# Kernel tuning notes

Hardware: AMD Instinct MI355X
Metric: run time of the kernel (lower is better)

## Reference

```python
import jax, jax.numpy as jnp
import numpy as np

N = 43
H = N // 2  # 21


def _mk(key, i, o):
    kw, kb = jax.random.split(key)
    bound = 1.0 / np.sqrt(i)
    W = jax.random.uniform(kw, (i, o), jnp.float32, -bound, bound)
    b = jax.random.uniform(kb, (o,), jnp.float32, -bound, bound)
    return W, b


def setup_inputs() -> dict:
    key = jax.random.key(0)
    keys = jax.random.split(key, 11)
    x = jax.random.normal(keys[0], (1048576, N), jnp.float32)
    dims = [(N, N), (N, N), (N, N), (N, N), (N, H),  # encoder
            (H, N), (N, N), (N, N), (N, N), (N, N)]  # decoder
    out = {"x": x}
    for li, (i, o) in enumerate(dims):
        W, b = _mk(keys[li + 1], i, o)
        out[f"W{li}"] = W
        out[f"b{li}"] = b
    return out


def reference(x, W0, b0, W1, b1, W2, b2, W3, b3, W4, b4,
              W5, b5, W6, b6, W7, b7, W8, b8, W9, b9):
    Ws = [W0, W1, W2, W3, W4, W5, W6, W7, W8, W9]
    bs = [b0, b1, b2, b3, b4, b5, b6, b7, b8, b9]
    h = x
    for li in range(10):
        h = h @ Ws[li] + bs[li]
        # tanh after every layer except encoder bottleneck (4) and final (9)
        if li not in (4, 9):
            h = jnp.tanh(h)
    return h
```

## Files before the change

### kernel.cpp

```cpp
#include <hip/hip_runtime.h>


typedef __fp16 pk16x2 __attribute__((ext_vector_type(2)));
typedef _Float16 f16x8 __attribute__((ext_vector_type(8)));
typedef float f32x4 __attribute__((ext_vector_type(4)));
typedef unsigned u32x4 __attribute__((ext_vector_type(4)));

#define TPB 1024
#define NBLK 256
#define ITERS 8
#define NROWS 1048576
#define NCOL 43
#define ROWB 172u
#define XBYTES ((size_t)NROWS * ROWB)
#define WSTRIDE 72
#define SLOT_ROWS 44
#define WSLOT (SLOT_ROWS * WSTRIDE)
#define W_BYTES (10 * WSLOT * 2)
#define XBUF_BYTES 6144
#define X_BASE W_BYTES
#define SMEM_BYTES (X_BASE + 16 * XBUF_BYTES + 64)

__device__ __forceinline__ float fast_tanh(float x) {
  float t = __builtin_amdgcn_exp2f(x * 2.8853900817779268f);
  float r = __builtin_amdgcn_rcpf(t + 1.0f);
  return __builtin_fmaf(-2.0f, r, 1.0f);
}

__device__ __forceinline__ unsigned pk2(float a, float b) {
  pk16x2 h = __builtin_amdgcn_cvt_pkrtz(a, b);
  return __builtin_bit_cast(unsigned, h);
}

struct FragsV { f16x8 s0c0, s0c1, s1c0, s1c1; };

template <int NT, int KC, bool DOTANH, int NLOUT, int KCN>
__device__ __forceinline__ FragsV layer_fwd(const _Float16* __restrict__ Wl,
                                            FragsV Bi, f32x4 Z, int g, int lr) {
  f16x8 Bv[2][2];
  Bv[0][0] = Bi.s0c0; Bv[0][1] = Bi.s0c1;
  Bv[1][0] = Bi.s1c0; Bv[1][1] = Bi.s1c1;

  f32x4 acc[3][2];
#pragma unroll
  for (int t = 0; t < NT; ++t) {
    f16x8 A = *(const f16x8*)(Wl + (16 * t + lr) * WSTRIDE + 8 * g);
#pragma unroll
    for (int s = 0; s < 2; ++s)
      acc[t][s] = __builtin_amdgcn_mfma_f32_16x16x32_f16(A, Bv[s][0], Z,
                                                         0, 0, 0);
  }
#pragma unroll
  for (int c = 1; c < KC; ++c)
#pragma unroll
    for (int t = 0; t < NT; ++t) {
      f16x8 A = *(const f16x8*)(Wl + (16 * t + lr) * WSTRIDE + 8 * g + 32 * c);
#pragma unroll
      for (int s = 0; s < 2; ++s)
        acc[t][s] = __builtin_amdgcn_mfma_f32_16x16x32_f16(A, Bv[s][c],
                                                           acc[t][s], 0, 0, 0);
    }

  f16x8 oc0[2], oc1[2];
#pragma unroll
  for (int s = 0; s < 2; ++s) {
    unsigned pk[3][2];
#pragma unroll
    for (int t = 0; t < NT; ++t) {
      float v[4];
#pragma unroll
      for (int r = 0; r < 4; ++r) {
        float u = acc[t][s][r];
        if (DOTANH) u = fast_tanh(u);
        if (t == (NLOUT >> 4)) {
          int col = 16 * t + 4 * g + r;
          u = (col == NLOUT) ? 1.0f : u;
        }
        v[r] = u;
      }
      pk[t][0] = pk2(v[0], v[1]);
      pk[t][1] = pk2(v[2], v[3]);
    }
    u32x4 d0 = {pk[0][0], pk[0][1], pk[1][0], pk[1][1]};
    oc0[s] = __builtin_bit_cast(f16x8, d0);
    if (KCN == 2) {
      u32x4 d1 = {pk[NT - 1][0], pk[NT - 1][1], 0u, 0u};
      oc1[s] = __builtin_bit_cast(f16x8, d1);
    } else {
      oc1[s] = oc0[s];
    }
  }
  FragsV O;
  O.s0c0 = oc0[0]; O.s0c1 = oc1[0];
  O.s1c0 = oc0[1]; O.s1c1 = oc1[1];
  return O;
}

extern "C" __global__ void __launch_bounds__(TPB)
ae_kernel(const float* __restrict__ x,
          const float* __restrict__ W0, const float* __restrict__ B0,
          const float* __restrict__ W1, const float* __restrict__ B1,
          const float* __restrict__ W2, const float* __restrict__ B2,
          const float* __restrict__ W3, const float* __restrict__ B3,
          const float* __restrict__ W4, const float* __restrict__ B4,
          const float* __restrict__ W5, const float* __restrict__ B5,
          const float* __restrict__ W6, const float* __restrict__ B6,
          const float* __restrict__ W7, const float* __restrict__ B7,
          const float* __restrict__ W8, const float* __restrict__ B8,
          const float* __restrict__ W9, const float* __restrict__ B9,
          float* __restrict__ out) {
  extern __shared__ char smem[];
  _Float16* lw = (_Float16*)smem;

  const int tid = threadIdx.x;
  const int wave = tid >> 6;
  const int lane = tid & 63;
  const int g = lane >> 4;
  const int lr = lane & 15;

  {
    const float* Wp[10] = {W0, W1, W2, W3, W4, W5, W6, W7, W8, W9};
    const float* Bp[10] = {B0, B1, B2, B3, B4, B5, B6, B7, B8, B9};
    const int KLs[10] = {43, 43, 43, 43, 43, 21, 43, 43, 43, 43};
    const int NLs[10] = {43, 43, 43, 43, 21, 43, 43, 43, 43, 43};
#pragma unroll
    for (int L = 0; L < 10; ++L) {
      const float* Wl = Wp[L];
      const float* Bl = Bp[L];
      const int KL = KLs[L], NL = NLs[L];
      for (int idx = tid; idx < SLOT_ROWS * 64; idx += TPB) {
        int n = idx >> 6, kp = idx & 63;
        float v = 0.0f;
        if (n < NL) {
          int c = kp >> 5, g2 = (kp >> 3) & 3, j = kp & 7;
          int F;
          if (L == 0) F = kp;
          else if (c == 0) F = 16 * (j >> 2) + 4 * g2 + (j & 3);
          else if (j < 4)  F = 32 + 4 * g2 + j;
          else             F = 63;
          if (F < KL) v = Wl[F * NL + n];
          else if (F == KL) v = Bl[n];
        }
        lw[L * WSLOT + n * WSTRIDE + kp] = (_Float16)v;
      }
    }
  }

  unsigned dmaoff[6];
#pragma unroll
  for (int i = 0; i < 6; ++i) {
    unsigned u = 64u * i + (unsigned)lane;
    dmaoff[i] = (u / 12u) * ROWB + (u % 12u) * 16u;
  }

  __syncthreads();

  const char* xc = (const char*)x;
  const char* xlim = xc + (XBYTES - 16);
  const unsigned blockbase = (unsigned)blockIdx.x * (ITERS * 512) + wave * 32;
  float* xb = (float*)(smem + X_BASE + wave * XBUF_BYTES);
  const f32x4 Z = {0.f, 0.f, 0.f, 0.f};

  {
    const char* base = xc + blockbase * ROWB;
#pragma unroll
    for (int i = 0; i < 6; ++i) {
      const char* src = base + dmaoff[i];
      src = (src > xlim) ? xlim : src;
      __builtin_amdgcn_global_load_lds(
          (const __attribute__((address_space(1))) void*)src,
          (__attribute__((address_space(3))) void*)((char*)xb + i * 1024),
          16, 0, 0);
    }
  }

#pragma unroll 1
  for (int it = 0; it < ITERS; ++it) {
    const unsigned row0 = blockbase + (unsigned)it * 512u;

    asm volatile("s_waitcnt vmcnt(0)" ::: "memory");

    FragsV B;
#pragma unroll
    for (int s = 0; s < 2; ++s) {
      const float* xr = xb + (16 * s + lr) * 48;
      f32x4 q0 = *(const f32x4*)(xr + 8 * g);
      f32x4 q1 = *(const f32x4*)(xr + 8 * g + 4);
      f32x4 q2 = *(const f32x4*)(xr + 32 + 8 * g);
      f32x4 q3 = *(const f32x4*)(xr + 36 + 8 * g);
      float e3 = (g == 1) ? 1.0f : q2[3];
      u32x4 d0 = {pk2(q0[0], q0[1]), pk2(q0[2], q0[3]),
                  pk2(q1[0], q1[1]), pk2(q1[2], q1[3])};
      u32x4 d1 = {pk2(q2[0], q2[1]), pk2(q2[2], e3),
                  pk2(q3[0], q3[1]), pk2(q3[2], q3[3])};
      if (s == 0) { B.s0c0 = __builtin_bit_cast(f16x8, d0);
                    B.s0c1 = __builtin_bit_cast(f16x8, d1); }
      else        { B.s1c0 = __builtin_bit_cast(f16x8, d0);
                    B.s1c1 = __builtin_bit_cast(f16x8, d1); }
    }

    asm volatile("s_waitcnt lgkmcnt(0)" ::: "memory");
    if (it + 1 < ITERS) {
      const char* base = xc + (row0 + 512u) * ROWB;
#pragma unroll
      for (int i = 0; i < 6; ++i) {
        const char* src = base + dmaoff[i];
        src = (src > xlim) ? xlim : src;
        __builtin_amdgcn_global_load_lds(
            (const __attribute__((address_space(1))) void*)src,
            (__attribute__((address_space(3))) void*)((char*)xb + i * 1024),
            16, 0, 0);
      }
    }

    B = layer_fwd<3, 2, true, 43, 2>(lw + 0 * WSLOT, B, Z, g, lr);
    B = layer_fwd<3, 2, true, 43, 2>(lw + 1 * WSLOT, B, Z, g, lr);
    B = layer_fwd<3, 2, true, 43, 2>(lw + 2 * WSLOT, B, Z, g, lr);
    B = layer_fwd<3, 2, true, 43, 2>(lw + 3 * WSLOT, B, Z, g, lr);
    B = layer_fwd<2, 2, false, 21, 1>(lw + 4 * WSLOT, B, Z, g, lr);
    B = layer_fwd<3, 1, true, 43, 2>(lw + 5 * WSLOT, B, Z, g, lr);
    B = layer_fwd<3, 2, true, 43, 2>(lw + 6 * WSLOT, B, Z, g, lr);
    B = layer_fwd<3, 2, true, 43, 2>(lw + 7 * WSLOT, B, Z, g, lr);
    B = layer_fwd<3, 2, true, 43, 2>(lw + 8 * WSLOT, B, Z, g, lr);

    {
      f16x8 Bv[2][2];
      Bv[0][0] = B.s0c0; Bv[0][1] = B.s0c1;
      Bv[1][0] = B.s1c0; Bv[1][1] = B.s1c1;
      f32x4 a9[3][2];
#pragma unroll
      for (int t = 0; t < 3; ++t) {
        f16x8 A = *(const f16x8*)(lw + 9 * WSLOT + (16 * t + lr) * WSTRIDE +
                                  8 * g);
#pragma unroll
        for (int s = 0; s < 2; ++s)
          a9[t][s] = __builtin_amdgcn_mfma_f32_16x16x32_f16(A, Bv[s][0], Z,
                                                            0, 0, 0);
      }
#pragma unroll
      for (int t = 0; t < 3; ++t) {
        f16x8 A = *(const f16x8*)(lw + 9 * WSLOT + (16 * t + lr) * WSTRIDE +
                                  8 * g + 32);
#pragma unroll
        for (int s = 0; s < 2; ++s)
          a9[t][s] = __builtin_amdgcn_mfma_f32_16x16x32_f16(A, Bv[s][1],
                                                            a9[t][s], 0, 0, 0);
      }
      char* ob = (char*)out + ((size_t)(row0 + lr) * ROWB + 16u * g);
#pragma unroll
      for (int t = 0; t < 3; ++t)
#pragma unroll
        for (int s = 0; s < 2; ++s)
#pragma unroll
          for (int r = 0; r < 4; ++r) {
            if (t < 2 || 4 * g + r < 11)
              *(float*)(ob + 2752 * s + 64 * t + 4 * r) = a9[t][s][r];
          }
    }
  }
}

extern "C" void kernel_launch(void* const* d_in, const int* in_sizes, int n_in,
                              void* d_out, int out_size, void* d_ws,
                              size_t ws_size, hipStream_t stream) {
  const float* x = (const float*)d_in[0];
  const float* W[10];
  const float* B[10];
  for (int i = 0; i < 10; ++i) {
    W[i] = (const float*)d_in[1 + 2 * i];
    B[i] = (const float*)d_in[2 + 2 * i];
  }
  (void)hipFuncSetAttribute(reinterpret_cast<const void*>(ae_kernel),
                            hipFuncAttributeMaxDynamicSharedMemorySize,
                            SMEM_BYTES);
  ae_kernel<<<dim3(NBLK), dim3(TPB), SMEM_BYTES, stream>>>(
      x, W[0], B[0], W[1], B[1], W[2], B[2], W[3], B[3], W[4], B[4],
      W[5], B[5], W[6], B[6], W[7], B[7], W[8], B[8], W[9], B[9],
      (float*)d_out);
}
```

Baseline: 137.5 us.

## Prefetch next layer's weight fragments from LDS and tighten the x staging layout

```diff
diff --git a/kernel.cpp b/kernel.cpp
--- a/kernel.cpp
+++ b/kernel.cpp
@@ -17,9 +17,11 @@
 #define SLOT_ROWS 44
 #define WSLOT (SLOT_ROWS * WSTRIDE)
 #define W_BYTES (10 * WSLOT * 2)
+#define W_PAD 640
+#define XROWF 44
 #define XBUF_BYTES 6144
-#define X_BASE W_BYTES
-#define SMEM_BYTES (X_BASE + 16 * XBUF_BYTES + 64)
+#define X_BASE (W_BYTES + W_PAD)
+#define SMEM_BYTES (X_BASE + 16 * XBUF_BYTES)
 
 __device__ __forceinline__ float fast_tanh(float x) {
   float t = __builtin_amdgcn_exp2f(x * 2.8853900817779268f);
@@ -33,33 +35,51 @@
 }
 
 struct FragsV { f16x8 s0c0, s0c1, s1c0, s1c1; };
+struct A6 { f16x8 m0, m1, m2, m3, m4, m5; };
+
+template <int NT, int KC>
+__device__ __forceinline__ A6 load_A(const _Float16* __restrict__ Wl,
+                                     int g, int lr) {
+  A6 a;
+  const _Float16* p = Wl + lr * WSTRIDE + 8 * g;
+  a.m0 = *(const f16x8*)(p);
+  if constexpr (NT > 1) a.m1 = *(const f16x8*)(p + 16 * WSTRIDE);
+  if constexpr (NT > 2) a.m2 = *(const f16x8*)(p + 32 * WSTRIDE);
+  if constexpr (KC > 1) {
+    a.m3 = *(const f16x8*)(p + 32);
+    if constexpr (NT > 1) a.m4 = *(const f16x8*)(p + 16 * WSTRIDE + 32);
+    if constexpr (NT > 2) a.m5 = *(const f16x8*)(p + 32 * WSTRIDE + 32);
+  }
+  return a;
+}
 
 template <int NT, int KC, bool DOTANH, int NLOUT, int KCN>
-__device__ __forceinline__ FragsV layer_fwd(const _Float16* __restrict__ Wl,
-                                            FragsV Bi, f32x4 Z, int g, int lr) {
-  f16x8 Bv[2][2];
-  Bv[0][0] = Bi.s0c0; Bv[0][1] = Bi.s0c1;
-  Bv[1][0] = Bi.s1c0; Bv[1][1] = Bi.s1c1;
+__device__ __forceinline__ FragsV layer_fwd(A6 a, FragsV Bi, f32x4 Z, int g) {
+  f16x8 Bv0[2] = {Bi.s0c0, Bi.s1c0};
+  f16x8 Bv1[2] = {Bi.s0c1, Bi.s1c1};
 
   f32x4 acc[3][2];
 #pragma unroll
-  for (int t = 0; t < NT; ++t) {
-    f16x8 A = *(const f16x8*)(Wl + (16 * t + lr) * WSTRIDE + 8 * g);
-#pragma unroll
-    for (int s = 0; s < 2; ++s)
-      acc[t][s] = __builtin_amdgcn_mfma_f32_16x16x32_f16(A, Bv[s][0], Z,
-                                                         0, 0, 0);
-  }
-#pragma unroll
-  for (int c = 1; c < KC; ++c)
-#pragma unroll
-    for (int t = 0; t < NT; ++t) {
-      f16x8 A = *(const f16x8*)(Wl + (16 * t + lr) * WSTRIDE + 8 * g + 32 * c);
-#pragma unroll
-      for (int s = 0; s < 2; ++s)
-        acc[t][s] = __builtin_amdgcn_mfma_f32_16x16x32_f16(A, Bv[s][c],
-                                                           acc[t][s], 0, 0, 0);
-    }
+  for (int s = 0; s < 2; ++s) {
+    acc[0][s] = __builtin_amdgcn_mfma_f32_16x16x32_f16(a.m0, Bv0[s], Z, 0, 0, 0);
+    if constexpr (NT > 1)
+      acc[1][s] = __builtin_amdgcn_mfma_f32_16x16x32_f16(a.m1, Bv0[s], Z, 0, 0, 0);
+    if constexpr (NT > 2)
+      acc[2][s] = __builtin_amdgcn_mfma_f32_16x16x32_f16(a.m2, Bv0[s], Z, 0, 0, 0);
+  }
+  if constexpr (KC > 1) {
+#pragma unroll
+    for (int s = 0; s < 2; ++s) {
+      acc[0][s] = __builtin_amdgcn_mfma_f32_16x16x32_f16(a.m3, Bv1[s],
+                                                         acc[0][s], 0, 0, 0);
+      if constexpr (NT > 1)
+        acc[1][s] = __builtin_amdgcn_mfma_f32_16x16x32_f16(a.m4, Bv1[s],
+                                                           acc[1][s], 0, 0, 0);
+      if constexpr (NT > 2)
+        acc[2][s] = __builtin_amdgcn_mfma_f32_16x16x32_f16(a.m5, Bv1[s],
+                                                           acc[2][s], 0, 0, 0);
+    }
+  }
 
   f16x8 oc0[2], oc1[2];
 #pragma unroll
@@ -96,7 +116,7 @@
   return O;
 }
 
-extern "C" __global__ void __launch_bounds__(TPB)
+extern "C" __global__ void __launch_bounds__(TPB, 4)
 ae_kernel(const float* __restrict__ x,
           const float* __restrict__ W0, const float* __restrict__ B0,
           const float* __restrict__ W1, const float* __restrict__ B1,
@@ -150,7 +170,7 @@
 #pragma unroll
   for (int i = 0; i < 6; ++i) {
     unsigned u = 64u * i + (unsigned)lane;
-    dmaoff[i] = (u / 12u) * ROWB + (u % 12u) * 16u;
+    dmaoff[i] = (u / 11u) * ROWB + (u % 11u) * 16u;
   }
 
   __syncthreads();
@@ -174,6 +194,8 @@
     }
   }
 
+  A6 a0c = load_A<3, 2>(lw + 0 * WSLOT, g, lr);
+
 #pragma unroll 1
   for (int it = 0; it < ITERS; ++it) {
     const unsigned row0 = blockbase + (unsigned)it * 512u;
@@ -183,7 +205,7 @@
     FragsV B;
 #pragma unroll
     for (int s = 0; s < 2; ++s) {
-      const float* xr = xb + (16 * s + lr) * 48;
+      const float* xr = xb + (16 * s + lr) * XROWF;
       f32x4 q0 = *(const f32x4*)(xr + 8 * g);
       f32x4 q1 = *(const f32x4*)(xr + 8 * g + 4);
       f32x4 q2 = *(const f32x4*)(xr + 32 + 8 * g);
@@ -213,38 +235,45 @@
       }
     }
 
-    B = layer_fwd<3, 2, true, 43, 2>(lw + 0 * WSLOT, B, Z, g, lr);
-    B = layer_fwd<3, 2, true, 43, 2>(lw + 1 * WSLOT, B, Z, g, lr);
-    B = layer_fwd<3, 2, true, 43, 2>(lw + 2 * WSLOT, B, Z, g, lr);
-    B = layer_fwd<3, 2, true, 43, 2>(lw + 3 * WSLOT, B, Z, g, lr);
-    B = layer_fwd<2, 2, false, 21, 1>(lw + 4 * WSLOT, B, Z, g, lr);
-    B = layer_fwd<3, 1, true, 43, 2>(lw + 5 * WSLOT, B, Z, g, lr);
-    B = layer_fwd<3, 2, true, 43, 2>(lw + 6 * WSLOT, B, Z, g, lr);
-    B = layer_fwd<3, 2, true, 43, 2>(lw + 7 * WSLOT, B, Z, g, lr);
-    B = layer_fwd<3, 2, true, 43, 2>(lw + 8 * WSLOT, B, Z, g, lr);
+    A6 a1v = load_A<3, 2>(lw + 1 * WSLOT, g, lr);
+    B = layer_fwd<3, 2, true, 43, 2>(a0c, B, Z, g);
+    A6 a2v = load_A<3, 2>(lw + 2 * WSLOT, g, lr);
+    B = layer_fwd<3, 2, true, 43, 2>(a1v, B, Z, g);
+    A6 a3v = load_A<3, 2>(lw + 3 * WSLOT, g, lr);
+    B = layer_fwd<3, 2, true, 43, 2>(a2v, B, Z, g);
+    A6 a4v = load_A<2, 2>(lw + 4 * WSLOT, g, lr);
+    B = layer_fwd<3, 2, true, 43, 2>(a3v, B, Z, g);
+    A6 a5v = load_A<3, 1>(lw + 5 * WSLOT, g, lr);
+    B = layer_fwd<2, 2, false, 21, 1>(a4v, B, Z, g);
+    A6 a6v = load_A<3, 2>(lw + 6 * WSLOT, g, lr);
+    B = layer_fwd<3, 1, true, 43, 2>(a5v, B, Z, g);
+    A6 a7v = load_A<3, 2>(lw + 7 * WSLOT, g, lr);
+    B = layer_fwd<3, 2, true, 43, 2>(a6v, B, Z, g);
+    A6 a8v = load_A<3, 2>(lw + 8 * WSLOT, g, lr);
+    B = layer_fwd<3, 2, true, 43, 2>(a7v, B, Z, g);
+    A6 a9v = load_A<3, 2>(lw + 9 * WSLOT, g, lr);
+    B = layer_fwd<3, 2, true, 43, 2>(a8v, B, Z, g);
+
+    a0c = load_A<3, 2>(lw + 0 * WSLOT, g, lr);
 
     {
-      f16x8 Bv[2][2];
-      Bv[0][0] = B.s0c0; Bv[0][1] = B.s0c1;
-      Bv[1][0] = B.s1c0; Bv[1][1] = B.s1c1;
+      f16x8 Bv0[2] = {B.s0c0, B.s1c0};
+      f16x8 Bv1[2] = {B.s0c1, B.s1c1};
       f32x4 a9[3][2];
 #pragma unroll
-      for (int t = 0; t < 3; ++t) {
-        f16x8 A = *(const f16x8*)(lw + 9 * WSLOT + (16 * t + lr) * WSTRIDE +
-                                  8 * g);
-#pragma unroll
-        for (int s = 0; s < 2; ++s)
-          a9[t][s] = __builtin_amdgcn_mfma_f32_16x16x32_f16(A, Bv[s][0], Z,
-                                                            0, 0, 0);
-      }
-#pragma unroll
-      for (int t = 0; t < 3; ++t) {
-        f16x8 A = *(const f16x8*)(lw + 9 * WSLOT + (16 * t + lr) * WSTRIDE +
-                                  8 * g + 32);
-#pragma unroll
-        for (int s = 0; s < 2; ++s)
-          a9[t][s] = __builtin_amdgcn_mfma_f32_16x16x32_f16(A, Bv[s][1],
-                                                            a9[t][s], 0, 0, 0);
+      for (int s = 0; s < 2; ++s) {
+        a9[0][s] = __builtin_amdgcn_mfma_f32_16x16x32_f16(a9v.m0, Bv0[s], Z,
+                                                          0, 0, 0);
+        a9[1][s] = __builtin_amdgcn_mfma_f32_16x16x32_f16(a9v.m1, Bv0[s], Z,
+                                                          0, 0, 0);
+        a9[2][s] = __builtin_amdgcn_mfma_f32_16x16x32_f16(a9v.m2, Bv0[s], Z,
+                                                          0, 0, 0);
+        a9[0][s] = __builtin_amdgcn_mfma_f32_16x16x32_f16(a9v.m3, Bv1[s],
+                                                          a9[0][s], 0, 0, 0);
+        a9[1][s] = __builtin_amdgcn_mfma_f32_16x16x32_f16(a9v.m4, Bv1[s],
+                                                          a9[1][s], 0, 0, 0);
+        a9[2][s] = __builtin_amdgcn_mfma_f32_16x16x32_f16(a9v.m5, Bv1[s],
+                                                          a9[2][s], 0, 0, 0);
       }
       char* ob = (char*)out + ((size_t)(row0 + lr) * ROWB + 16u * g);
 #pragma unroll
```

New measurement: 135.9 us. No clear change (-1.2%).
